# Optimization experiments

Measured on AMD Instinct MI355X. Metric: run time of the kernel, lower is better.

Reference implementation:

```python
import jax, jax.numpy as jnp
import numpy as np

B, T, P, D, S, R = 4, 128, 256, 512, 64, 8  # batch, window, patches, d_model, n_state, dt_rank


def setup_inputs() -> dict:
    key = jax.random.key(0)
    ks = jax.random.split(key, 8)
    sc = 0.02  # weight init scale
    return {
        "X": jax.random.normal(ks[0], (B, T, P, D), jnp.float32),
        "H0": jnp.zeros((B, P, S), jnp.float32),
        "a_hat": jax.random.normal(ks[1], (S,), jnp.float32),
        "U_w": jax.random.normal(ks[2], (S, D), jnp.float32) * sc,
        "sB_w": jax.random.normal(ks[3], (S, D), jnp.float32) * sc,
        "sB_b": jnp.zeros((S,), jnp.float32),
        "sC_w": jax.random.normal(ks[4], (S, D), jnp.float32) * sc,
        "sC_b": jnp.zeros((S,), jnp.float32),
        "sD1_w": jax.random.normal(ks[5], (R, D), jnp.float32) * sc,
        "sD1_b": jnp.zeros((R,), jnp.float32),
        "sD2_w": jax.random.normal(ks[6], (1, R), jnp.float32) * sc,
        "sD2_b": jnp.zeros((1,), jnp.float32),
        "ro_w": jax.random.normal(ks[7], (D, S), jnp.float32) * sc,
    }


def reference(X, H0, a_hat, U_w, sB_w, sB_b, sC_w, sC_b, sD1_w, sD1_b, sD2_w, sD2_b, ro_w):
    eps = 1e-12
    logA = -jnp.exp(a_hat)                                    # [S]
    # selective (input-dependent) parameters
    u = jnp.einsum('btpd,sd->btps', X, U_w)                   # [B,T,P,S]
    B_t = jnp.einsum('btpd,sd->btps', X, sB_w) + sB_b
    C_t = jnp.einsum('btpd,sd->btps', X, sC_w) + sC_b
    dt_feat = jax.nn.silu(jnp.einsum('btpd,rd->btpr', X, sD1_w) + sD1_b)
    dt = jax.nn.softplus(jnp.einsum('btpr,or->btpo', dt_feat, sD2_w) + sD2_b)  # [B,T,P,1]
    A = jnp.exp(dt * logA)                                    # [B,T,P,S] via broadcast
    b = (1.0 - A) * (B_t * u)
    # prefix-product scan: h_t = A_t*h_{t-1} + b_t  ->  h_t = P_t*(H0 + cumsum(b/P))
    Pc = jnp.cumprod(jnp.maximum(A, eps), axis=1)             # [B,T,P,S]
    invP = 1.0 / jnp.maximum(Pc, eps)
    c = jnp.cumsum(b * invP, axis=1)
    H_seq = Pc * (H0[:, None] + c)                            # [B,T,P,S]
    Y_seq = jnp.einsum('btps,ds->btpd', C_t * H_seq, ro_w)    # [B,T,P,D]
    Y_seq = Y_seq.reshape(X.shape[0], -1, X.shape[-1])        # [B, T*P, D]
    H_T = H_seq[:, -1]                                        # [B,P,S]
    return (H_seq, Y_seq, H_T)
```

## Files before the change

### kernel.cpp

```cpp
#include <hip/hip_runtime.h>
#include <hip/hip_bf16.h>
#include <math.h>

namespace {
constexpr int B_N = 4, T_N = 128, P_N = 256, D_N = 512, S_N = 64;
constexpr int NTH = 512;
constexpr int KC  = 32;
constexpr int NCH = D_N / KC;

constexpr int XS0_OFF = 0;
constexpr int WS0_OFF = 8192;
constexpr int XS1_OFF = 21504;
constexpr int WS1_OFF = 29696;
constexpr int BU_OFF  = 0;
constexpr int CH_OFF  = 16384;
constexpr int ROS_OFF = 0;
constexpr int DT_OFF  = 43008;
constexpr int LDS_BYTES = 43520;
}

typedef short bf16x8 __attribute__((ext_vector_type(8)));
typedef float f32x4  __attribute__((ext_vector_type(4)));

__device__ __forceinline__ unsigned short f2b(float f) {
    unsigned int x = __float_as_uint(f);
    return (unsigned short)((x + 0x7FFFu + ((x >> 16) & 1u)) >> 16);
}
__device__ __forceinline__ float b2f(unsigned short h) {
    return __uint_as_float(((unsigned int)h) << 16);
}
__device__ __forceinline__ unsigned int pk2(float lo, float hi) {
    union { __hip_bfloat162 h; unsigned int u; } cv;
    cv.h = __float22bfloat162_rn(float2{lo, hi});
    return cv.u;
}
__device__ __forceinline__ int swz32(int row, int col) {
    return row * 32 + (col ^ (((row >> 1) & 3) << 3));
}
__device__ __forceinline__ int swz64(int row, int col) {
    return row * 64 + (col ^ ((row & 7) << 3));
}
__device__ __forceinline__ void cvtstore8(unsigned short* dst, float4 a, float4 b) {
    uint4 r;
    r.x = pk2(a.x, a.y); r.y = pk2(a.z, a.w);
    r.z = pk2(b.x, b.y); r.w = pk2(b.z, b.w);
    *(uint4*)dst = r;
}

__global__ __launch_bounds__(NTH, 4) void mamba_mfma(
    const float* __restrict__ X, const float* __restrict__ H0,
    const float* __restrict__ a_hat,
    const float* __restrict__ U_w, const float* __restrict__ sB_w, const float* __restrict__ sB_b,
    const float* __restrict__ sC_w, const float* __restrict__ sC_b,
    const float* __restrict__ sD1_w, const float* __restrict__ sD1_b,
    const float* __restrict__ sD2_w, const float* __restrict__ sD2_b,
    const float* __restrict__ ro_w,
    float* __restrict__ Hseq, float* __restrict__ Y, float* __restrict__ HT)
{
    __shared__ __align__(16) char smem[LDS_BYTES];
    unsigned short* XS0 = (unsigned short*)(smem + XS0_OFF);
    unsigned short* WS0 = (unsigned short*)(smem + WS0_OFF);
    unsigned short* XS1 = (unsigned short*)(smem + XS1_OFF);
    unsigned short* WS1 = (unsigned short*)(smem + WS1_OFF);
    unsigned short* BU  = (unsigned short*)(smem + BU_OFF);
    unsigned short* ROS = (unsigned short*)(smem + ROS_OFF);
    unsigned short* CHB = (unsigned short*)(smem + CH_OFF);
    float*          DTB = (float*)(smem + DT_OFF);

    const int tid  = threadIdx.x;
    const int lane = tid & 63;
    const int wid  = tid >> 6;
    const int wm   = wid >> 2;
    const int wn   = wid & 3;
    const int l15  = lane & 15;
    const int lg   = lane >> 4;
    const int b    = blockIdx.x >> 8;
    const int p    = blockIdx.x & 255;

    const float la  = (tid < 64) ? -expf(a_hat[tid]) : 0.0f;
    const float h0v = (tid < 64) ? H0[((size_t)b * P_N + p) * S_N + tid] : 0.0f;

    if (tid < 128) {
        ((unsigned int*)(WS0 + 200 * 32))[tid] = 0;
        ((unsigned int*)(WS1 + 200 * 32))[tid] = 0;
    }

    f32x4 acc[4][3];
    f32x4 accdt;
    #pragma unroll
    for (int q = 0; q < 4; ++q) accdt[q] = 0.0f;
    #pragma unroll
    for (int mf = 0; mf < 4; ++mf)
        #pragma unroll
        for (int nf = 0; nf < 3; ++nf)
            #pragma unroll
            for (int q = 0; q < 4; ++q) acc[mf][nf][q] = 0.0f;

    const int xr = tid >> 2, xq = tid & 3;
    const float* xsrc = X + (((size_t)b * T_N + xr) * P_N + p) * D_N + xq * 8;
    const int xoff = swz32(xr, xq * 8);

    const int wr0 = tid >> 2, wq = tid & 3;
    const int wr1 = 128 + wr0;
    const bool hasW1 = (tid < 288);
    const float* wsrc0;
    {
        int g = wr0 >> 4, w = wr0 & 15, tr = g % 3, sb = g / 3;
        const float* base = (tr == 0) ? U_w : (tr == 1) ? sB_w : sC_w;
        wsrc0 = base + (size_t)(sb * 16 + w) * D_N + wq * 8;
    }
    const float* wsrc1;
    if (wr1 < 192) {
        int g = wr1 >> 4, w = wr1 & 15, tr = g % 3, sb = g / 3;
        const float* base = (tr == 0) ? U_w : (tr == 1) ? sB_w : sC_w;
        wsrc1 = base + (size_t)(sb * 16 + w) * D_N + wq * 8;
    } else if (wr1 < 200) {
        wsrc1 = sD1_w + (size_t)(wr1 - 192) * D_N + wq * 8;
    } else {
        wsrc1 = wsrc0;
    }
    const int woff0 = swz32(wr0, wq * 8);
    const int woff1 = swz32(wr1 < 208 ? wr1 : 0, wq * 8);

    float4 xA = *(const float4*)(xsrc),   xB = *(const float4*)(xsrc + 4);
    float4 wA0 = *(const float4*)(wsrc0), wB0 = *(const float4*)(wsrc0 + 4);
    float4 wA1 = *(const float4*)(wsrc1), wB1 = *(const float4*)(wsrc1 + 4);
    cvtstore8(&XS0[xoff],  xA, xB);
    cvtstore8(&WS0[woff0], wA0, wB0);
    if (hasW1) cvtstore8(&WS0[woff1], wA1, wB1);
    {
        const float* nx = xsrc + KC;
        xA = *(const float4*)(nx); xB = *(const float4*)(nx + 4);
        const float* n0 = wsrc0 + KC;
        wA0 = *(const float4*)(n0); wB0 = *(const float4*)(n0 + 4);
        const float* n1 = wsrc1 + KC;
        wA1 = *(const float4*)(n1); wB1 = *(const float4*)(n1 + 4);
    }
    __syncthreads();

    const int kb = lg * 8;
    #pragma unroll 2
    for (int kc = 0; kc < NCH; ++kc) {
        unsigned short* XSc = (kc & 1) ? XS1 : XS0;
        unsigned short* WSc = (kc & 1) ? WS1 : WS0;
        unsigned short* XSn = (kc & 1) ? XS0 : XS1;
        unsigned short* WSn = (kc & 1) ? WS0 : WS1;
        if (kc + 1 < NCH) {
            cvtstore8(&XSn[xoff],  xA, xB);
            cvtstore8(&WSn[woff0], wA0, wB0);
            if (hasW1) cvtstore8(&WSn[woff1], wA1, wB1);
        }
        if (kc + 2 < NCH) {
            const float* nx = xsrc + (kc + 2) * KC;
            xA = *(const float4*)(nx); xB = *(const float4*)(nx + 4);
            const float* n0 = wsrc0 + (kc + 2) * KC;
            wA0 = *(const float4*)(n0); wB0 = *(const float4*)(n0 + 4);
            const float* n1 = wsrc1 + (kc + 2) * KC;
            wA1 = *(const float4*)(n1); wB1 = *(const float4*)(n1 + 4);
        }
        __builtin_amdgcn_s_setprio(1);
        bf16x8 a[4];
        #pragma unroll
        for (int mf = 0; mf < 4; ++mf)
            a[mf] = *(const bf16x8*)&XSc[swz32(wm * 64 + mf * 16 + l15, kb)];
        #pragma unroll
        for (int nf = 0; nf < 3; ++nf) {
            bf16x8 bb = *(const bf16x8*)&WSc[swz32(wn * 48 + nf * 16 + l15, kb)];
            #pragma unroll
            for (int mf = 0; mf < 4; ++mf)
                acc[mf][nf] = __builtin_amdgcn_mfma_f32_16x16x32_bf16(a[mf], bb, acc[mf][nf], 0, 0, 0);
        }
        {
            bf16x8 adt = *(const bf16x8*)&XSc[swz32(wid * 16 + l15, kb)];
            bf16x8 bd  = *(const bf16x8*)&WSc[swz32(192 + l15, kb)];
            accdt = __builtin_amdgcn_mfma_f32_16x16x32_bf16(adt, bd, accdt, 0, 0, 0);
        }
        __builtin_amdgcn_s_setprio(0);
        __syncthreads();
    }

    {
        const int s = wn * 16 + l15;
        const float biasB = sB_b[s], biasC = sC_b[s];
        #pragma unroll
        for (int mf = 0; mf < 4; ++mf) {
            #pragma unroll
            for (int q = 0; q < 4; ++q) {
                const int t = wm * 64 + mf * 16 + lg * 4 + q;
                const float u  = acc[mf][0][q];
                const float Bv = acc[mf][1][q] + biasB;
                const float Cv = acc[mf][2][q] + biasC;
                BU[t * 64 + s]   = f2b(Bv * u);
                CHB[swz64(t, s)] = f2b(Cv);
            }
        }
    }
    {
        const float w2 = (l15 < 8) ? sD2_w[l15] : 0.0f;
        const float b1 = (l15 < 8) ? sD1_b[l15] : 0.0f;
        const float b2 = sD2_b[0];
        #pragma unroll
        for (int q = 0; q < 4; ++q) {
            float z = accdt[q] + b1;
            float w = (z / (1.0f + expf(-z))) * w2;
            w = (l15 < 8) ? w : 0.0f;
            w += __shfl_xor(w, 1);
            w += __shfl_xor(w, 2);
            w += __shfl_xor(w, 4);
            if (l15 == 0) {
                float zz = w + b2;
                DTB[wid * 16 + lg * 4 + q] = (zz > 20.0f) ? zz : log1pf(expf(zz));
            }
        }
    }
    __syncthreads();

    const int rrow = tid >> 2, rq = tid & 3;
    const float* rosrc = ro_w + (size_t)rrow * S_N + rq * 16;
    float4 r0a = *(const float4*)(rosrc);
    float4 r0b = *(const float4*)(rosrc + 4);
    float4 r0c = *(const float4*)(rosrc + 8);
    float4 r0d = *(const float4*)(rosrc + 12);

    if (tid < 64) {
        const int s = tid;
        float Pcv = 1.0f, cv = 0.0f, Hv = 0.0f;
        float* hout = Hseq + ((size_t)b * T_N * P_N + p) * S_N + s;
        for (int t = 0; t < T_N; ++t) {
            const float Av = expf(DTB[t] * la);
            const float bv = (1.0f - Av) * b2f(BU[t * 64 + s]);
            Pcv *= fmaxf(Av, 1e-12f);
            cv += bv * (1.0f / fmaxf(Pcv, 1e-12f));
            Hv = Pcv * (h0v + cv);
            hout[(size_t)t * P_N * S_N] = Hv;
            const int e = swz64(t, s);
            CHB[e] = f2b(b2f(CHB[e]) * Hv);
        }
        HT[((size_t)b * P_N + p) * S_N + s] = Hv;
    }
    __syncthreads();

    bf16x8 af0[4], af1[4];
    #pragma unroll
    for (int mf = 0; mf < 4; ++mf) {
        af0[mf] = *(const bf16x8*)&CHB[swz64(wm * 64 + mf * 16 + l15, lg * 8)];
        af1[mf] = *(const bf16x8*)&CHB[swz64(wm * 64 + mf * 16 + l15, 32 + lg * 8)];
    }
    cvtstore8(&ROS[swz64(rrow, rq * 16)],     r0a, r0b);
    cvtstore8(&ROS[swz64(rrow, rq * 16 + 8)], r0c, r0d);
    __syncthreads();

    for (int pp = 0; pp < 4; ++pp) {
        if (pp < 3) {
            const float* ns = ro_w + (size_t)((pp + 1) * 128 + rrow) * S_N + rq * 16;
            r0a = *(const float4*)(ns);
            r0b = *(const float4*)(ns + 4);
            r0c = *(const float4*)(ns + 8);
            r0d = *(const float4*)(ns + 12);
        }
        f32x4 yacc[4][2];
        #pragma unroll
        for (int mf = 0; mf < 4; ++mf)
            #pragma unroll
            for (int nf = 0; nf < 2; ++nf)
                #pragma unroll
                for (int q = 0; q < 4; ++q) yacc[mf][nf][q] = 0.0f;
        #pragma unroll
        for (int nf = 0; nf < 2; ++nf) {
            bf16x8 bb0 = *(const bf16x8*)&ROS[swz64(wn * 32 + nf * 16 + l15, lg * 8)];
            bf16x8 bb1 = *(const bf16x8*)&ROS[swz64(wn * 32 + nf * 16 + l15, 32 + lg * 8)];
            #pragma unroll
            for (int mf = 0; mf < 4; ++mf) {
                yacc[mf][nf] = __builtin_amdgcn_mfma_f32_16x16x32_bf16(af0[mf], bb0, yacc[mf][nf], 0, 0, 0);
                yacc[mf][nf] = __builtin_amdgcn_mfma_f32_16x16x32_bf16(af1[mf], bb1, yacc[mf][nf], 0, 0, 0);
            }
        }
        #pragma unroll
        for (int mf = 0; mf < 4; ++mf) {
            const int t0 = wm * 64 + mf * 16 + lg * 4;
            float* ybase = Y + (((size_t)b * T_N + t0) * P_N + p) * D_N + pp * 128 + wn * 32 + l15;
            #pragma unroll
            for (int nf = 0; nf < 2; ++nf) {
                #pragma unroll
                for (int q = 0; q < 4; ++q)
                    ybase[(size_t)q * P_N * D_N + nf * 16] = yacc[mf][nf][q];
            }
        }
        __syncthreads();
        if (pp < 3) {
            cvtstore8(&ROS[swz64(rrow, rq * 16)],     r0a, r0b);
            cvtstore8(&ROS[swz64(rrow, rq * 16 + 8)], r0c, r0d);
            __syncthreads();
        }
    }
}

extern "C" void kernel_launch(void* const* d_in, const int* in_sizes, int n_in,
                              void* d_out, int out_size, void* d_ws, size_t ws_size,
                              hipStream_t stream) {
    const float* X     = (const float*)d_in[0];
    const float* H0    = (const float*)d_in[1];
    const float* a_hat = (const float*)d_in[2];
    const float* U_w   = (const float*)d_in[3];
    const float* sB_w  = (const float*)d_in[4];
    const float* sB_b  = (const float*)d_in[5];
    const float* sC_w  = (const float*)d_in[6];
    const float* sC_b  = (const float*)d_in[7];
    const float* sD1_w = (const float*)d_in[8];
    const float* sD1_b = (const float*)d_in[9];
    const float* sD2_w = (const float*)d_in[10];
    const float* sD2_b = (const float*)d_in[11];
    const float* ro_w  = (const float*)d_in[12];

    float* out   = (float*)d_out;
    float* HseqP = out;
    float* YP    = out + (size_t)B_N * T_N * P_N * S_N;
    float* HTP   = YP  + (size_t)B_N * T_N * P_N * D_N;

    hipLaunchKernelGGL(mamba_mfma, dim3(B_N * P_N), dim3(NTH), 0, stream,
                       X, H0, a_hat, U_w, sB_w, sB_b, sC_w, sC_b,
                       sD1_w, sD1_b, sD2_w, sD2_b, ro_w, HseqP, YP, HTP);
}
```

Baseline: 156.5 us.

## Split fused Mamba kernel into projection, scan, and output GEMM kernels

Replaces the single fused per-(batch,patch) kernel with three kernels: a row-tiled projection GEMM that writes B*u, C (bf16) and dt to workspace, a per-(b,p) 64-thread scan producing H_seq and C*H, and a row-tiled GEMM against ro_w for Y. The aim is better parallelism and coalescing, since the fused kernel processes a strided (b,p) column over time. The cost is extra global round trips through workspace, two more launches, and a scan kernel with only 64 threads per block and strided element loads. The fused kernel is kept as a fallback when the workspace is too small.

```diff
diff --git a/kernel.cpp b/kernel.cpp
--- a/kernel.cpp
+++ b/kernel.cpp
@@ -7,16 +7,27 @@
 constexpr int NTH = 512;
 constexpr int KC  = 32;
 constexpr int NCH = D_N / KC;
+constexpr size_t NROWS = (size_t)B_N * T_N * P_N;
 
 constexpr int XS0_OFF = 0;
 constexpr int WS0_OFF = 8192;
 constexpr int XS1_OFF = 21504;
 constexpr int WS1_OFF = 29696;
-constexpr int BU_OFF  = 0;
-constexpr int CH_OFF  = 16384;
+constexpr int K1_LDS  = 43008;
+
 constexpr int ROS_OFF = 0;
-constexpr int DT_OFF  = 43008;
-constexpr int LDS_BYTES = 43520;
+constexpr int CH3_OFF = 16384;
+constexpr int K3_LDS  = 32768;
+
+constexpr int FXS0_OFF = 0;
+constexpr int FWS0_OFF = 8192;
+constexpr int FXS1_OFF = 21504;
+constexpr int FWS1_OFF = 29696;
+constexpr int FBU_OFF  = 0;
+constexpr int FCH_OFF  = 16384;
+constexpr int FROS_OFF = 0;
+constexpr int FDT_OFF  = 43008;
+constexpr int F_LDS    = 43520;
 }
 
 typedef short bf16x8 __attribute__((ext_vector_type(8)));
@@ -47,7 +58,306 @@
     *(uint4*)dst = r;
 }
 
-__global__ __launch_bounds__(NTH, 4) void mamba_mfma(
+__global__ __launch_bounds__(NTH, 4) void mamba_proj(
+    const float* __restrict__ X,
+    const float* __restrict__ U_w, const float* __restrict__ sB_w, const float* __restrict__ sB_b,
+    const float* __restrict__ sC_w, const float* __restrict__ sC_b,
+    const float* __restrict__ sD1_w, const float* __restrict__ sD1_b,
+    const float* __restrict__ sD2_w, const float* __restrict__ sD2_b,
+    unsigned short* __restrict__ BUCH, unsigned short* __restrict__ CG,
+    float* __restrict__ DTW)
+{
+    __shared__ __align__(16) char smem[K1_LDS];
+    unsigned short* XS0 = (unsigned short*)(smem + XS0_OFF);
+    unsigned short* WS0 = (unsigned short*)(smem + WS0_OFF);
+    unsigned short* XS1 = (unsigned short*)(smem + XS1_OFF);
+    unsigned short* WS1 = (unsigned short*)(smem + WS1_OFF);
+
+    const int tid  = threadIdx.x;
+    const int lane = tid & 63;
+    const int wid  = tid >> 6;
+    const int wm   = wid >> 2;
+    const int wn   = wid & 3;
+    const int l15  = lane & 15;
+    const int lg   = lane >> 4;
+    const size_t row0 = (size_t)blockIdx.x * 128;
+
+    if (tid < 128) {
+        ((unsigned int*)(WS0 + 200 * 32))[tid] = 0;
+        ((unsigned int*)(WS1 + 200 * 32))[tid] = 0;
+    }
+
+    f32x4 acc[4][3];
+    f32x4 accdt;
+    #pragma unroll
+    for (int q = 0; q < 4; ++q) accdt[q] = 0.0f;
+    #pragma unroll
+    for (int mf = 0; mf < 4; ++mf)
+        #pragma unroll
+        for (int nf = 0; nf < 3; ++nf)
+            #pragma unroll
+            for (int q = 0; q < 4; ++q) acc[mf][nf][q] = 0.0f;
+
+    const int xr = tid >> 2, xq = tid & 3;
+    const float* xsrc = X + (row0 + xr) * D_N + xq * 8;
+    const int xoff = swz32(xr, xq * 8);
+
+    const int wr0 = tid >> 2, wq = tid & 3;
+    const int wr1 = 128 + wr0;
+    const bool hasW1 = (tid < 288);
+    const float* wsrc0;
+    {
+        int g = wr0 >> 4, w = wr0 & 15, tr = g % 3, sb = g / 3;
+        const float* base = (tr == 0) ? U_w : (tr == 1) ? sB_w : sC_w;
+        wsrc0 = base + (size_t)(sb * 16 + w) * D_N + wq * 8;
+    }
+    const float* wsrc1;
+    if (wr1 < 192) {
+        int g = wr1 >> 4, w = wr1 & 15, tr = g % 3, sb = g / 3;
+        const float* base = (tr == 0) ? U_w : (tr == 1) ? sB_w : sC_w;
+        wsrc1 = base + (size_t)(sb * 16 + w) * D_N + wq * 8;
+    } else if (wr1 < 200) {
+        wsrc1 = sD1_w + (size_t)(wr1 - 192) * D_N + wq * 8;
+    } else {
+        wsrc1 = wsrc0;
+    }
+    const int woff0 = swz32(wr0, wq * 8);
+    const int woff1 = swz32(wr1 < 208 ? wr1 : 0, wq * 8);
+
+    float4 xA = *(const float4*)(xsrc),   xB = *(const float4*)(xsrc + 4);
+    float4 wA0 = *(const float4*)(wsrc0), wB0 = *(const float4*)(wsrc0 + 4);
+    float4 wA1 = *(const float4*)(wsrc1), wB1 = *(const float4*)(wsrc1 + 4);
+    cvtstore8(&XS0[xoff],  xA, xB);
+    cvtstore8(&WS0[woff0], wA0, wB0);
+    if (hasW1) cvtstore8(&WS0[woff1], wA1, wB1);
+    {
+        const float* nx = xsrc + KC;
+        xA = *(const float4*)(nx); xB = *(const float4*)(nx + 4);
+        const float* n0 = wsrc0 + KC;
+        wA0 = *(const float4*)(n0); wB0 = *(const float4*)(n0 + 4);
+        const float* n1 = wsrc1 + KC;
+        wA1 = *(const float4*)(n1); wB1 = *(const float4*)(n1 + 4);
+    }
+    __syncthreads();
+
+    const int kb = lg * 8;
+    #pragma unroll 2
+    for (int kc = 0; kc < NCH; ++kc) {
+        unsigned short* XSc = (kc & 1) ? XS1 : XS0;
+        unsigned short* WSc = (kc & 1) ? WS1 : WS0;
+        unsigned short* XSn = (kc & 1) ? XS0 : XS1;
+        unsigned short* WSn = (kc & 1) ? WS0 : WS1;
+        if (kc + 1 < NCH) {
+            cvtstore8(&XSn[xoff],  xA, xB);
+            cvtstore8(&WSn[woff0], wA0, wB0);
+            if (hasW1) cvtstore8(&WSn[woff1], wA1, wB1);
+        }
+        if (kc + 2 < NCH) {
+            const float* nx = xsrc + (kc + 2) * KC;
+            xA = *(const float4*)(nx); xB = *(const float4*)(nx + 4);
+            const float* n0 = wsrc0 + (kc + 2) * KC;
+            wA0 = *(const float4*)(n0); wB0 = *(const float4*)(n0 + 4);
+            const float* n1 = wsrc1 + (kc + 2) * KC;
+            wA1 = *(const float4*)(n1); wB1 = *(const float4*)(n1 + 4);
+        }
+        __builtin_amdgcn_s_setprio(1);
+        bf16x8 a[4];
+        #pragma unroll
+        for (int mf = 0; mf < 4; ++mf)
+            a[mf] = *(const bf16x8*)&XSc[swz32(wm * 64 + mf * 16 + l15, kb)];
+        #pragma unroll
+        for (int nf = 0; nf < 3; ++nf) {
+            bf16x8 bb = *(const bf16x8*)&WSc[swz32(wn * 48 + nf * 16 + l15, kb)];
+            #pragma unroll
+            for (int mf = 0; mf < 4; ++mf)
+                acc[mf][nf] = __builtin_amdgcn_mfma_f32_16x16x32_bf16(a[mf], bb, acc[mf][nf], 0, 0, 0);
+        }
+        {
+            bf16x8 adt = *(const bf16x8*)&XSc[swz32(wid * 16 + l15, kb)];
+            bf16x8 bd  = *(const bf16x8*)&WSc[swz32(192 + l15, kb)];
+            accdt = __builtin_amdgcn_mfma_f32_16x16x32_bf16(adt, bd, accdt, 0, 0, 0);
+        }
+        __builtin_amdgcn_s_setprio(0);
+        __syncthreads();
+    }
+
+    {
+        const int s = wn * 16 + l15;
+        const float biasB = sB_b[s], biasC = sC_b[s];
+        #pragma unroll
+        for (int mf = 0; mf < 4; ++mf) {
+            #pragma unroll
+            for (int q = 0; q < 4; ++q) {
+                const size_t r = row0 + wm * 64 + mf * 16 + lg * 4 + q;
+                const float u  = acc[mf][0][q];
+                const float Bv = acc[mf][1][q] + biasB;
+                const float Cv = acc[mf][2][q] + biasC;
+                BUCH[r * 64 + s] = f2b(Bv * u);
+                CG[r * 64 + s]   = f2b(Cv);
+            }
+        }
+    }
+    {
+        const float w2 = (l15 < 8) ? sD2_w[l15] : 0.0f;
+        const float b1 = (l15 < 8) ? sD1_b[l15] : 0.0f;
+        const float b2 = sD2_b[0];
+        #pragma unroll
+        for (int q = 0; q < 4; ++q) {
+            float z = accdt[q] + b1;
+            float w = (z / (1.0f + expf(-z))) * w2;
+            w = (l15 < 8) ? w : 0.0f;
+            w += __shfl_xor(w, 1);
+            w += __shfl_xor(w, 2);
+            w += __shfl_xor(w, 4);
+            if (l15 == 0) {
+                float zz = w + b2;
+                DTW[row0 + wid * 16 + lg * 4 + q] = (zz > 20.0f) ? zz : log1pf(expf(zz));
+            }
+        }
+    }
+}
+
+__global__ __launch_bounds__(64, 8) void mamba_scan(
+    const float* __restrict__ H0, const float* __restrict__ a_hat,
+    unsigned short* __restrict__ BUCH, const unsigned short* __restrict__ CG,
+    const float* __restrict__ DTW,
+    float* __restrict__ Hseq, float* __restrict__ HT)
+{
+    const int blk = blockIdx.x;
+    const int b = blk >> 8, p = blk & 255;
+    const int s = threadIdx.x;
+    const size_t base = (size_t)b * T_N * P_N + p;
+    const size_t i0 = base * 64 + s;
+
+    const float la  = -expf(a_hat[s]);
+    const float h0v = H0[((size_t)b * P_N + p) * S_N + s];
+    float Pcv = 1.0f, cv = 0.0f, Hv = 0.0f;
+
+    float bu[4], cc[4], dtq[4];
+    #pragma unroll
+    for (int q = 0; q < 4; ++q) {
+        const size_t ix = i0 + (size_t)q * (P_N * 64);
+        bu[q]  = b2f(BUCH[ix]);
+        cc[q]  = b2f(CG[ix]);
+        dtq[q] = DTW[base + (size_t)q * P_N];
+    }
+    for (int t0 = 0; t0 < T_N; t0 += 4) {
+        float nbu[4], ncc[4], ndt[4];
+        if (t0 + 4 < T_N) {
+            #pragma unroll
+            for (int q = 0; q < 4; ++q) {
+                const size_t ix = i0 + (size_t)(t0 + 4 + q) * (P_N * 64);
+                nbu[q] = b2f(BUCH[ix]);
+                ncc[q] = b2f(CG[ix]);
+                ndt[q] = DTW[base + (size_t)(t0 + 4 + q) * P_N];
+            }
+        }
+        #pragma unroll
+        for (int q = 0; q < 4; ++q) {
+            const int t = t0 + q;
+            const float Av = expf(dtq[q] * la);
+            const float bv = (1.0f - Av) * bu[q];
+            Pcv *= fmaxf(Av, 1e-12f);
+            cv += bv * (1.0f / fmaxf(Pcv, 1e-12f));
+            Hv = Pcv * (h0v + cv);
+            const size_t ix = i0 + (size_t)t * (P_N * 64);
+            Hseq[ix] = Hv;
+            BUCH[ix] = f2b(cc[q] * Hv);
+        }
+        #pragma unroll
+        for (int q = 0; q < 4; ++q) { bu[q] = nbu[q]; cc[q] = ncc[q]; dtq[q] = ndt[q]; }
+    }
+    HT[((size_t)b * P_N + p) * S_N + s] = Hv;
+}
+
+__global__ __launch_bounds__(NTH, 4) void mamba_ygemm(
+    const unsigned short* __restrict__ CHG, const float* __restrict__ ro_w,
+    float* __restrict__ Y)
+{
+    __shared__ __align__(16) char smem[K3_LDS];
+    unsigned short* ROS = (unsigned short*)(smem + ROS_OFF);
+    unsigned short* CHB = (unsigned short*)(smem + CH3_OFF);
+
+    const int tid  = threadIdx.x;
+    const int lane = tid & 63;
+    const int wid  = tid >> 6;
+    const int wm   = wid >> 2;
+    const int wn   = wid & 3;
+    const int l15  = lane & 15;
+    const int lg   = lane >> 4;
+    const size_t row0 = (size_t)blockIdx.x * 128;
+
+    const int crow = tid >> 2, cq = tid & 3;
+    {
+        const uint4 v0 = *(const uint4*)(CHG + (row0 + crow) * 64 + cq * 16);
+        const uint4 v1 = *(const uint4*)(CHG + (row0 + crow) * 64 + cq * 16 + 8);
+        *(uint4*)&CHB[swz64(crow, cq * 16)]     = v0;
+        *(uint4*)&CHB[swz64(crow, cq * 16 + 8)] = v1;
+    }
+    const int rrow = tid >> 2, rq = tid & 3;
+    const float* rosrc = ro_w + (size_t)rrow * S_N + rq * 16;
+    float4 r0a = *(const float4*)(rosrc);
+    float4 r0b = *(const float4*)(rosrc + 4);
+    float4 r0c = *(const float4*)(rosrc + 8);
+    float4 r0d = *(const float4*)(rosrc + 12);
+    __syncthreads();
+
+    bf16x8 af0[4], af1[4];
+    #pragma unroll
+    for (int mf = 0; mf < 4; ++mf) {
+        af0[mf] = *(const bf16x8*)&CHB[swz64(wm * 64 + mf * 16 + l15, lg * 8)];
+        af1[mf] = *(const bf16x8*)&CHB[swz64(wm * 64 + mf * 16 + l15, 32 + lg * 8)];
+    }
+    cvtstore8(&ROS[swz64(rrow, rq * 16)],     r0a, r0b);
+    cvtstore8(&ROS[swz64(rrow, rq * 16 + 8)], r0c, r0d);
+    __syncthreads();
+
+    for (int pp = 0; pp < 4; ++pp) {
+        if (pp < 3) {
+            const float* ns = ro_w + (size_t)((pp + 1) * 128 + rrow) * S_N + rq * 16;
+            r0a = *(const float4*)(ns);
+            r0b = *(const float4*)(ns + 4);
+            r0c = *(const float4*)(ns + 8);
+            r0d = *(const float4*)(ns + 12);
+        }
+        f32x4 yacc[4][2];
+        #pragma unroll
+        for (int mf = 0; mf < 4; ++mf)
+            #pragma unroll
+            for (int nf = 0; nf < 2; ++nf)
+                #pragma unroll
+                for (int q = 0; q < 4; ++q) yacc[mf][nf][q] = 0.0f;
+        #pragma unroll
+        for (int nf = 0; nf < 2; ++nf) {
+            bf16x8 bb0 = *(const bf16x8*)&ROS[swz64(wn * 32 + nf * 16 + l15, lg * 8)];
+            bf16x8 bb1 = *(const bf16x8*)&ROS[swz64(wn * 32 + nf * 16 + l15, 32 + lg * 8)];
+            #pragma unroll
+            for (int mf = 0; mf < 4; ++mf) {
+                yacc[mf][nf] = __builtin_amdgcn_mfma_f32_16x16x32_bf16(af0[mf], bb0, yacc[mf][nf], 0, 0, 0);
+                yacc[mf][nf] = __builtin_amdgcn_mfma_f32_16x16x32_bf16(af1[mf], bb1, yacc[mf][nf], 0, 0, 0);
+            }
+        }
+        #pragma unroll
+        for (int mf = 0; mf < 4; ++mf) {
+            const size_t r = row0 + wm * 64 + mf * 16 + lg * 4;
+            float* ybase = Y + r * D_N + pp * 128 + wn * 32 + l15;
+            #pragma unroll
+            for (int nf = 0; nf < 2; ++nf) {
+                #pragma unroll
+                for (int q = 0; q < 4; ++q)
+                    ybase[(size_t)q * D_N + nf * 16] = yacc[mf][nf][q];
+            }
+        }
+        __syncthreads();
+        if (pp < 3) {
+            cvtstore8(&ROS[swz64(rrow, rq * 16)],     r0a, r0b);
+            cvtstore8(&ROS[swz64(rrow, rq * 16 + 8)], r0c, r0d);
+            __syncthreads();
+        }
+    }
+}
+
+__global__ __launch_bounds__(NTH, 4) void mamba_fused(
     const float* __restrict__ X, const float* __restrict__ H0,
     const float* __restrict__ a_hat,
     const float* __restrict__ U_w, const float* __restrict__ sB_w, const float* __restrict__ sB_b,
@@ -57,15 +367,15 @@
     const float* __restrict__ ro_w,
     float* __restrict__ Hseq, float* __restrict__ Y, float* __restrict__ HT)
 {
-    __shared__ __align__(16) char smem[LDS_BYTES];
-    unsigned short* XS0 = (unsigned short*)(smem + XS0_OFF);
-    unsigned short* WS0 = (unsigned short*)(smem + WS0_OFF);
-    unsigned short* XS1 = (unsigned short*)(smem + XS1_OFF);
-    unsigned short* WS1 = (unsigned short*)(smem + WS1_OFF);
-    unsigned short* BU  = (unsigned short*)(smem + BU_OFF);
-    unsigned short* ROS = (unsigned short*)(smem + ROS_OFF);
-    unsigned short* CHB = (unsigned short*)(smem + CH_OFF);
-    float*          DTB = (float*)(smem + DT_OFF);
+    __shared__ __align__(16) char smem[F_LDS];
+    unsigned short* XS0 = (unsigned short*)(smem + FXS0_OFF);
+    unsigned short* WS0 = (unsigned short*)(smem + FWS0_OFF);
+    unsigned short* XS1 = (unsigned short*)(smem + FXS1_OFF);
+    unsigned short* WS1 = (unsigned short*)(smem + FWS1_OFF);
+    unsigned short* BU  = (unsigned short*)(smem + FBU_OFF);
+    unsigned short* ROS = (unsigned short*)(smem + FROS_OFF);
+    unsigned short* CHB = (unsigned short*)(smem + FCH_OFF);
+    float*          DTB = (float*)(smem + FDT_OFF);
 
     const int tid  = threadIdx.x;
     const int lane = tid & 63;
@@ -317,7 +627,24 @@
     float* YP    = out + (size_t)B_N * T_N * P_N * S_N;
     float* HTP   = YP  + (size_t)B_N * T_N * P_N * D_N;
 
-    hipLaunchKernelGGL(mamba_mfma, dim3(B_N * P_N), dim3(NTH), 0, stream,
-                       X, H0, a_hat, U_w, sB_w, sB_b, sC_w, sC_b,
-                       sD1_w, sD1_b, sD2_w, sD2_b, ro_w, HseqP, YP, HTP);
-}
+    const size_t buBytes = NROWS * 64 * 2;
+    const size_t wsNeed  = 2 * buBytes + NROWS * 4;
+
+    if (ws_size >= wsNeed) {
+        unsigned short* BUCH = (unsigned short*)d_ws;
+        unsigned short* CG   = (unsigned short*)((char*)d_ws + buBytes);
+        float*          DTW  = (float*)((char*)d_ws + 2 * buBytes);
+
+        hipLaunchKernelGGL(mamba_proj, dim3(1024), dim3(NTH), 0, stream,
+                           X, U_w, sB_w, sB_b, sC_w, sC_b,
+                           sD1_w, sD1_b, sD2_w, sD2_b, BUCH, CG, DTW);
+        hipLaunchKernelGGL(mamba_scan, dim3(1024), dim3(64), 0, stream,
+                           H0, a_hat, BUCH, CG, DTW, HseqP, HTP);
+        hipLaunchKernelGGL(mamba_ygemm, dim3(1024), dim3(NTH), 0, stream,
+                           BUCH, ro_w, YP);
+    } else {
+        hipLaunchKernelGGL(mamba_fused, dim3(B_N * P_N), dim3(NTH), 0, stream,
+                           X, H0, a_hat, U_w, sB_w, sB_b, sC_w, sC_b,
+                           sD1_w, sD1_b, sD2_w, sD2_b, ro_w, HseqP, YP, HTP);
+    }
+}
```

Measured after the change: 180.4 us. 15.3% more time.

## Pre-convert weights to swizzled bf16 images in a prep kernel

Applied to the files above, without the earlier changes.

Adds a prep kernel that converts the projection and readout weights to bf16 once, already padded and laid out in the swizzled LDS format, into a workspace buffer. The main kernel then copies the weight tiles into shared memory with plain 16-byte loads, with no per-block fp32-to-bf16 conversion and half the global weight traffic. The readout weights get double-buffered LDS tiles: the first is loaded during the serial scan and the rest are prefetched during the Y MFMAs, which removes one barrier per readout step. The cost is an extra kernel launch, workspace use, and a larger LDS footprint that may reduce occupancy.

```diff
diff --git a/kernel.cpp b/kernel.cpp
--- a/kernel.cpp
+++ b/kernel.cpp
@@ -10,13 +10,17 @@
 
 constexpr int XS0_OFF = 0;
 constexpr int WS0_OFF = 8192;
-constexpr int XS1_OFF = 21504;
-constexpr int WS1_OFF = 29696;
+constexpr int XS1_OFF = 24576;
+constexpr int WS1_OFF = 32768;
 constexpr int BU_OFF  = 0;
 constexpr int CH_OFF  = 16384;
-constexpr int ROS_OFF = 0;
-constexpr int DT_OFF  = 43008;
-constexpr int LDS_BYTES = 43520;
+constexpr int ROS0_OFF= 32768;
+constexpr int ROS1_OFF= 0;
+constexpr int DT_OFF  = 49152;
+constexpr int LDS_BYTES = 49664;
+
+constexpr int WIMG_ELEMS  = NCH * 256 * 32;
+constexpr int ROIMG_ELEMS = 4 * 128 * 64;
 }
 
 typedef short bf16x8 __attribute__((ext_vector_type(8)));
@@ -47,25 +51,42 @@
     *(uint4*)dst = r;
 }
 
+__global__ __launch_bounds__(512) void mamba_prep(
+    const float* __restrict__ U_w, const float* __restrict__ sB_w,
+    const float* __restrict__ sC_w, const float* __restrict__ sD1_w,
+    const float* __restrict__ ro_w,
+    unsigned short* __restrict__ wImg, unsigned short* __restrict__ roImg)
+{
+    const int idx = blockIdx.x * 512 + threadIdx.x;
+    if (idx < WIMG_ELEMS) {
+        const int kc = idx >> 13, rem = idx & 8191, r = rem >> 5, c = rem & 31;
+        float v = 0.0f;
+        if (r < 192) {
+            const int g = r >> 4, w = r & 15, tr = g % 3, sb = g / 3;
+            const float* base = (tr == 0) ? U_w : (tr == 1) ? sB_w : sC_w;
+            v = base[(size_t)(sb * 16 + w) * D_N + kc * KC + c];
+        } else if (r < 200) {
+            v = sD1_w[(size_t)(r - 192) * D_N + kc * KC + c];
+        }
+        wImg[kc * 8192 + swz32(r, c)] = f2b(v);
+    } else if (idx < WIMG_ELEMS + ROIMG_ELEMS) {
+        const int j = idx - WIMG_ELEMS;
+        const int pp = j >> 13, rem = j & 8191, r = rem >> 6, c = rem & 63;
+        roImg[pp * 8192 + swz64(r, c)] = f2b(ro_w[(size_t)(pp * 128 + r) * S_N + c]);
+    }
+}
+
 __global__ __launch_bounds__(NTH, 4) void mamba_mfma(
     const float* __restrict__ X, const float* __restrict__ H0,
     const float* __restrict__ a_hat,
-    const float* __restrict__ U_w, const float* __restrict__ sB_w, const float* __restrict__ sB_b,
-    const float* __restrict__ sC_w, const float* __restrict__ sC_b,
-    const float* __restrict__ sD1_w, const float* __restrict__ sD1_b,
-    const float* __restrict__ sD2_w, const float* __restrict__ sD2_b,
-    const float* __restrict__ ro_w,
+    const float* __restrict__ sB_b, const float* __restrict__ sC_b,
+    const float* __restrict__ sD1_b, const float* __restrict__ sD2_w,
+    const float* __restrict__ sD2_b,
+    const unsigned short* __restrict__ wImg, const unsigned short* __restrict__ roImg,
     float* __restrict__ Hseq, float* __restrict__ Y, float* __restrict__ HT)
 {
     __shared__ __align__(16) char smem[LDS_BYTES];
-    unsigned short* XS0 = (unsigned short*)(smem + XS0_OFF);
-    unsigned short* WS0 = (unsigned short*)(smem + WS0_OFF);
-    unsigned short* XS1 = (unsigned short*)(smem + XS1_OFF);
-    unsigned short* WS1 = (unsigned short*)(smem + WS1_OFF);
-    unsigned short* BU  = (unsigned short*)(smem + BU_OFF);
-    unsigned short* ROS = (unsigned short*)(smem + ROS_OFF);
-    unsigned short* CHB = (unsigned short*)(smem + CH_OFF);
-    float*          DTB = (float*)(smem + DT_OFF);
+    float* DTB = (float*)(smem + DT_OFF);
 
     const int tid  = threadIdx.x;
     const int lane = tid & 63;
@@ -80,11 +101,6 @@
     const float la  = (tid < 64) ? -expf(a_hat[tid]) : 0.0f;
     const float h0v = (tid < 64) ? H0[((size_t)b * P_N + p) * S_N + tid] : 0.0f;
 
-    if (tid < 128) {
-        ((unsigned int*)(WS0 + 200 * 32))[tid] = 0;
-        ((unsigned int*)(WS1 + 200 * 32))[tid] = 0;
-    }
-
     f32x4 acc[4][3];
     f32x4 accdt;
     #pragma unroll
@@ -100,63 +116,39 @@
     const float* xsrc = X + (((size_t)b * T_N + xr) * P_N + p) * D_N + xq * 8;
     const int xoff = swz32(xr, xq * 8);
 
-    const int wr0 = tid >> 2, wq = tid & 3;
-    const int wr1 = 128 + wr0;
-    const bool hasW1 = (tid < 288);
-    const float* wsrc0;
-    {
-        int g = wr0 >> 4, w = wr0 & 15, tr = g % 3, sb = g / 3;
-        const float* base = (tr == 0) ? U_w : (tr == 1) ? sB_w : sC_w;
-        wsrc0 = base + (size_t)(sb * 16 + w) * D_N + wq * 8;
-    }
-    const float* wsrc1;
-    if (wr1 < 192) {
-        int g = wr1 >> 4, w = wr1 & 15, tr = g % 3, sb = g / 3;
-        const float* base = (tr == 0) ? U_w : (tr == 1) ? sB_w : sC_w;
-        wsrc1 = base + (size_t)(sb * 16 + w) * D_N + wq * 8;
-    } else if (wr1 < 200) {
-        wsrc1 = sD1_w + (size_t)(wr1 - 192) * D_N + wq * 8;
-    } else {
-        wsrc1 = wsrc0;
-    }
-    const int woff0 = swz32(wr0, wq * 8);
-    const int woff1 = swz32(wr1 < 208 ? wr1 : 0, wq * 8);
-
-    float4 xA = *(const float4*)(xsrc),   xB = *(const float4*)(xsrc + 4);
-    float4 wA0 = *(const float4*)(wsrc0), wB0 = *(const float4*)(wsrc0 + 4);
-    float4 wA1 = *(const float4*)(wsrc1), wB1 = *(const float4*)(wsrc1 + 4);
-    cvtstore8(&XS0[xoff],  xA, xB);
-    cvtstore8(&WS0[woff0], wA0, wB0);
-    if (hasW1) cvtstore8(&WS0[woff1], wA1, wB1);
+    const char* wImgB = (const char*)wImg;
+
+    float4 xA = *(const float4*)(xsrc), xB = *(const float4*)(xsrc + 4);
+    uint4 wpA = *((const uint4*)(wImgB) + tid * 2);
+    uint4 wpB = *((const uint4*)(wImgB) + tid * 2 + 1);
+    cvtstore8((unsigned short*)(smem + XS0_OFF) + xoff, xA, xB);
+    *((uint4*)(smem + WS0_OFF) + tid * 2)     = wpA;
+    *((uint4*)(smem + WS0_OFF) + tid * 2 + 1) = wpB;
     {
         const float* nx = xsrc + KC;
         xA = *(const float4*)(nx); xB = *(const float4*)(nx + 4);
-        const float* n0 = wsrc0 + KC;
-        wA0 = *(const float4*)(n0); wB0 = *(const float4*)(n0 + 4);
-        const float* n1 = wsrc1 + KC;
-        wA1 = *(const float4*)(n1); wB1 = *(const float4*)(n1 + 4);
+        wpA = *((const uint4*)(wImgB + 16384) + tid * 2);
+        wpB = *((const uint4*)(wImgB + 16384) + tid * 2 + 1);
     }
     __syncthreads();
 
     const int kb = lg * 8;
     #pragma unroll 2
     for (int kc = 0; kc < NCH; ++kc) {
-        unsigned short* XSc = (kc & 1) ? XS1 : XS0;
-        unsigned short* WSc = (kc & 1) ? WS1 : WS0;
-        unsigned short* XSn = (kc & 1) ? XS0 : XS1;
-        unsigned short* WSn = (kc & 1) ? WS0 : WS1;
+        unsigned short* XSc = (unsigned short*)(smem + ((kc & 1) ? XS1_OFF : XS0_OFF));
+        unsigned short* WSc = (unsigned short*)(smem + ((kc & 1) ? WS1_OFF : WS0_OFF));
+        char*           XSn = smem + ((kc & 1) ? XS0_OFF : XS1_OFF);
+        char*           WSn = smem + ((kc & 1) ? WS0_OFF : WS1_OFF);
         if (kc + 1 < NCH) {
-            cvtstore8(&XSn[xoff],  xA, xB);
-            cvtstore8(&WSn[woff0], wA0, wB0);
-            if (hasW1) cvtstore8(&WSn[woff1], wA1, wB1);
+            cvtstore8((unsigned short*)XSn + xoff, xA, xB);
+            *((uint4*)WSn + tid * 2)     = wpA;
+            *((uint4*)WSn + tid * 2 + 1) = wpB;
         }
         if (kc + 2 < NCH) {
             const float* nx = xsrc + (kc + 2) * KC;
             xA = *(const float4*)(nx); xB = *(const float4*)(nx + 4);
-            const float* n0 = wsrc0 + (kc + 2) * KC;
-            wA0 = *(const float4*)(n0); wB0 = *(const float4*)(n0 + 4);
-            const float* n1 = wsrc1 + (kc + 2) * KC;
-            wA1 = *(const float4*)(n1); wB1 = *(const float4*)(n1 + 4);
+            wpA = *((const uint4*)(wImgB + (kc + 2) * 16384) + tid * 2);
+            wpB = *((const uint4*)(wImgB + (kc + 2) * 16384) + tid * 2 + 1);
         }
         __builtin_amdgcn_s_setprio(1);
         bf16x8 a[4];
@@ -180,6 +172,8 @@
     }
 
     {
+        unsigned short* BU  = (unsigned short*)(smem + BU_OFF);
+        unsigned short* CHB = (unsigned short*)(smem + CH_OFF);
         const int s = wn * 16 + l15;
         const float biasB = sB_b[s], biasC = sC_b[s];
         #pragma unroll
@@ -215,14 +209,9 @@
     }
     __syncthreads();
 
-    const int rrow = tid >> 2, rq = tid & 3;
-    const float* rosrc = ro_w + (size_t)rrow * S_N + rq * 16;
-    float4 r0a = *(const float4*)(rosrc);
-    float4 r0b = *(const float4*)(rosrc + 4);
-    float4 r0c = *(const float4*)(rosrc + 8);
-    float4 r0d = *(const float4*)(rosrc + 12);
-
     if (tid < 64) {
+        unsigned short* BU  = (unsigned short*)(smem + BU_OFF);
+        unsigned short* CHB = (unsigned short*)(smem + CH_OFF);
         const int s = tid;
         float Pcv = 1.0f, cv = 0.0f, Hv = 0.0f;
         float* hout = Hseq + ((size_t)b * T_N * P_N + p) * S_N + s;
@@ -237,26 +226,33 @@
             CHB[e] = f2b(b2f(CHB[e]) * Hv);
         }
         HT[((size_t)b * P_N + p) * S_N + s] = Hv;
+    } else {
+        for (int u = tid - 64; u < 512; u += 448) {
+            uint4 a0 = *((const uint4*)roImg + u * 2);
+            uint4 a1 = *((const uint4*)roImg + u * 2 + 1);
+            *((uint4*)(smem + ROS0_OFF) + u * 2)     = a0;
+            *((uint4*)(smem + ROS0_OFF) + u * 2 + 1) = a1;
+        }
     }
     __syncthreads();
 
     bf16x8 af0[4], af1[4];
-    #pragma unroll
-    for (int mf = 0; mf < 4; ++mf) {
-        af0[mf] = *(const bf16x8*)&CHB[swz64(wm * 64 + mf * 16 + l15, lg * 8)];
-        af1[mf] = *(const bf16x8*)&CHB[swz64(wm * 64 + mf * 16 + l15, 32 + lg * 8)];
-    }
-    cvtstore8(&ROS[swz64(rrow, rq * 16)],     r0a, r0b);
-    cvtstore8(&ROS[swz64(rrow, rq * 16 + 8)], r0c, r0d);
-    __syncthreads();
+    {
+        unsigned short* CHB = (unsigned short*)(smem + CH_OFF);
+        #pragma unroll
+        for (int mf = 0; mf < 4; ++mf) {
+            af0[mf] = *(const bf16x8*)&CHB[swz64(wm * 64 + mf * 16 + l15, lg * 8)];
+            af1[mf] = *(const bf16x8*)&CHB[swz64(wm * 64 + mf * 16 + l15, 32 + lg * 8)];
+        }
+    }
 
     for (int pp = 0; pp < 4; ++pp) {
+        unsigned short* cur = (unsigned short*)(smem + ((pp & 1) ? ROS1_OFF : ROS0_OFF));
+        char*           nxt = smem + ((pp & 1) ? ROS0_OFF : ROS1_OFF);
+        uint4 npA, npB;
         if (pp < 3) {
-            const float* ns = ro_w + (size_t)((pp + 1) * 128 + rrow) * S_N + rq * 16;
-            r0a = *(const float4*)(ns);
-            r0b = *(const float4*)(ns + 4);
-            r0c = *(const float4*)(ns + 8);
-            r0d = *(const float4*)(ns + 12);
+            const uint4* s = (const uint4*)((const char*)roImg + (pp + 1) * 16384) + tid * 2;
+            npA = s[0]; npB = s[1];
         }
         f32x4 yacc[4][2];
         #pragma unroll
@@ -267,13 +263,17 @@
                 for (int q = 0; q < 4; ++q) yacc[mf][nf][q] = 0.0f;
         #pragma unroll
         for (int nf = 0; nf < 2; ++nf) {
-            bf16x8 bb0 = *(const bf16x8*)&ROS[swz64(wn * 32 + nf * 16 + l15, lg * 8)];
-            bf16x8 bb1 = *(const bf16x8*)&ROS[swz64(wn * 32 + nf * 16 + l15, 32 + lg * 8)];
+            bf16x8 bb0 = *(const bf16x8*)&cur[swz64(wn * 32 + nf * 16 + l15, lg * 8)];
+            bf16x8 bb1 = *(const bf16x8*)&cur[swz64(wn * 32 + nf * 16 + l15, 32 + lg * 8)];
             #pragma unroll
             for (int mf = 0; mf < 4; ++mf) {
                 yacc[mf][nf] = __builtin_amdgcn_mfma_f32_16x16x32_bf16(af0[mf], bb0, yacc[mf][nf], 0, 0, 0);
                 yacc[mf][nf] = __builtin_amdgcn_mfma_f32_16x16x32_bf16(af1[mf], bb1, yacc[mf][nf], 0, 0, 0);
             }
+        }
+        if (pp < 3) {
+            *((uint4*)nxt + tid * 2)     = npA;
+            *((uint4*)nxt + tid * 2 + 1) = npB;
         }
         #pragma unroll
         for (int mf = 0; mf < 4; ++mf) {
@@ -286,12 +286,7 @@
                     ybase[(size_t)q * P_N * D_N + nf * 16] = yacc[mf][nf][q];
             }
         }
-        __syncthreads();
-        if (pp < 3) {
-            cvtstore8(&ROS[swz64(rrow, rq * 16)],     r0a, r0b);
-            cvtstore8(&ROS[swz64(rrow, rq * 16 + 8)], r0c, r0d);
-            __syncthreads();
-        }
+        if (pp < 3) __syncthreads();
     }
 }
 
@@ -317,7 +312,12 @@
     float* YP    = out + (size_t)B_N * T_N * P_N * S_N;
     float* HTP   = YP  + (size_t)B_N * T_N * P_N * D_N;
 
+    unsigned short* wImg  = (unsigned short*)d_ws;
+    unsigned short* roImg = (unsigned short*)((char*)d_ws + 262144);
+
+    hipLaunchKernelGGL(mamba_prep, dim3((WIMG_ELEMS + ROIMG_ELEMS) / 512), dim3(512), 0, stream,
+                       U_w, sB_w, sC_w, sD1_w, ro_w, wImg, roImg);
     hipLaunchKernelGGL(mamba_mfma, dim3(B_N * P_N), dim3(NTH), 0, stream,
-                       X, H0, a_hat, U_w, sB_w, sB_b, sC_w, sC_b,
-                       sD1_w, sD1_b, sD2_w, sD2_b, ro_w, HseqP, YP, HTP);
-}
+                       X, H0, a_hat, sB_b, sC_b, sD1_b, sD2_w, sD2_b,
+                       wImg, roImg, HseqP, YP, HTP);
+}
```

Result: no change. 153.7 us (-1.7%).
